# Performance work log

Hardware: AMD Instinct MI355X
Metric: run time of the kernel (lower is better)

Reference implementation:

```python
import jax, jax.numpy as jnp
import numpy as np

E = 2048   # embed_dim
H = 16     # num query heads
D = E // H # head_dim = 128
B = 2
S = 2048


def setup_inputs() -> dict:
    key = jax.random.key(0)
    ks = jax.random.split(key, 12)
    sc = 0.02
    return {
        "input": jax.random.normal(ks[0], (B, S, E), jnp.float32),
        "kv": jax.random.normal(ks[1], (B, S, E), jnp.float32),
        "Wq": jax.random.normal(ks[2], (E, E), jnp.float32) * sc,
        "bq": jnp.zeros((E,), jnp.float32),
        "Wk": jax.random.normal(ks[3], (D, E), jnp.float32) * sc,
        "bk": jnp.zeros((D,), jnp.float32),
        "Wv": jax.random.normal(ks[4], (D, E), jnp.float32) * sc,
        "bv": jnp.zeros((D,), jnp.float32),
        "Wo": jax.random.normal(ks[5], (E, E), jnp.float32) * sc,
        "bo": jnp.zeros((E,), jnp.float32),
        "expanding_context": 0,
    }


def reference(input, kv, Wq, bq, Wk, bk, Wv, bv, Wo, bo, expanding_context):
    b, s, _ = input.shape
    # projections (torch Linear: x @ W.T + b)
    q = (input @ Wq.T + bq).reshape(b, s, H, D).transpose(0, 2, 1, 3)  # [B,H,S,D]
    k = kv @ Wk.T + bk  # [B,S,D] single KV head
    v = kv @ Wv.T + bv  # [B,S,D]
    # scores with single KV head broadcast across query heads
    scores = jnp.einsum('bhsd,btd->bhst', q, k) / jnp.sqrt(jnp.float32(D))
    causal = jnp.triu(jnp.ones((s, s), bool), k=1)  # True above diagonal
    scores = jnp.where(causal[None, None], jnp.float32(-jnp.inf), scores)
    attn = jax.nn.softmax(scores, axis=-1)
    out = jnp.einsum('bhst,btd->bhsd', attn, v)  # [B,H,S,D]
    out = out.transpose(0, 2, 1, 3).reshape(b, s, E)
    return out @ Wo.T + bo
```

## Files before the change

### kernel.cpp

```cpp
#include <hip/hip_runtime.h>

#define B_  2
#define S_  2048
#define E_  2048
#define H_  16
#define D_  128
#define BS_ (B_*S_)

typedef __bf16 bf16_t;
typedef __bf16 bf16x8 __attribute__((ext_vector_type(8)));
typedef __bf16 bf16x4 __attribute__((ext_vector_type(4)));
typedef float  f32x4  __attribute__((ext_vector_type(4)));
typedef float  f32x16 __attribute__((ext_vector_type(16)));

#define QSCALE 0.1275174131003543f

__device__ __forceinline__ void gld16(const bf16_t* g, bf16_t* l) {
    __builtin_amdgcn_global_load_lds(
        (const __attribute__((address_space(1))) void*)g,
        (__attribute__((address_space(3))) void*)l,
        16, 0, 0);
}

__global__ void cvt_all(const float* __restrict__ s0, const float* __restrict__ s1,
                        const float* __restrict__ s2, const float* __restrict__ s3,
                        const float* __restrict__ s4, const float* __restrict__ s5,
                        bf16_t* d0, bf16_t* d1, bf16_t* d2,
                        bf16_t* d3, bf16_t* d4, bf16_t* d5)
{
    long i = ((long)blockIdx.x * blockDim.x + threadIdx.x) * 4;
    const float* s; bf16_t* d;
    if      (i <  8388608) { s = s0; d = d0; }
    else if (i < 16777216) { s = s1; d = d1; i -=  8388608; }
    else if (i < 20971520) { s = s2; d = d2; i -= 16777216; }
    else if (i < 21233664) { s = s3; d = d3; i -= 20971520; }
    else if (i < 21495808) { s = s4; d = d4; i -= 21233664; }
    else                   { s = s5; d = d5; i -= 21495808; }
    float4 v = *(const float4*)(s + i);
    bf16x4 o;
    o[0] = (bf16_t)v.x; o[1] = (bf16_t)v.y; o[2] = (bf16_t)v.z; o[3] = (bf16_t)v.w;
    *(bf16x4*)(d + i) = o;
}

template<int EP>
__device__ __forceinline__ void gemm_tile128(
    const bf16_t* __restrict__ A, const bf16_t* __restrict__ W,
    const float* __restrict__ bias,
    bf16_t* __restrict__ Cb,
    int N, int K, int kb, int ke, float scale, int m0, int w_n0, int c_n0,
    bf16_t* As, bf16_t* Bs)
{
    const int tid  = threadIdx.x;
    const int wave = tid >> 6, lane = tid & 63;
    const int wm = wave >> 1, wn = wave & 1;
    const int lrow = lane & 15, quad = lane >> 4;
    const int r8 = lane >> 3, c8 = (lane & 7) << 3;

    f32x4 acc[4][4] = {};

    for (int k0 = kb; k0 < ke; k0 += 64) {
        __syncthreads();
#pragma unroll
        for (int j = 0; j < 4; ++j) {
            int base = (wave * 4 + j) * 8;
            gld16(A + (size_t)(m0 + base + r8) * K + k0 + c8, &As[base * 64]);
        }
#pragma unroll
        for (int j = 0; j < 4; ++j) {
            int base = (wave * 4 + j) * 8;
            gld16(W + (size_t)(w_n0 + base + r8) * K + k0 + c8, &Bs[base * 64]);
        }
        __syncthreads();
#pragma unroll
        for (int ks = 0; ks < 2; ++ks) {
            bf16x8 af[4], bfr[4];
#pragma unroll
            for (int mt = 0; mt < 4; ++mt)
                af[mt] = *(const bf16x8*)&As[(wm * 64 + mt * 16 + lrow) * 64 + ks * 32 + quad * 8];
#pragma unroll
            for (int nt = 0; nt < 4; ++nt)
                bfr[nt] = *(const bf16x8*)&Bs[(wn * 64 + nt * 16 + lrow) * 64 + ks * 32 + quad * 8];
#pragma unroll
            for (int mt = 0; mt < 4; ++mt)
#pragma unroll
                for (int nt = 0; nt < 4; ++nt)
                    acc[mt][nt] = __builtin_amdgcn_mfma_f32_16x16x32_bf16(
                        af[mt], bfr[nt], acc[mt][nt], 0, 0, 0);
        }
    }

#pragma unroll
    for (int mt = 0; mt < 4; ++mt) {
#pragma unroll
        for (int nt = 0; nt < 4; ++nt) {
            int lcol = wn * 64 + nt * 16 + lrow;
            int col = c_n0 + lcol;
            float bvv = (EP == 1) ? bias[lcol] : 0.f;
#pragma unroll
            for (int r = 0; r < 4; ++r) {
                int row = m0 + wm * 64 + mt * 16 + quad * 4 + r;
                float v = (EP == 1) ? (acc[mt][nt][r] + bvv) * scale
                                    : acc[mt][nt][r];
                Cb[(size_t)row * N + col] = (bf16_t)v;
            }
        }
    }
}

__global__ __launch_bounds__(256) void gemm_qkv(
    const bf16_t* __restrict__ xb, const bf16_t* __restrict__ kvb,
    const bf16_t* __restrict__ Wq, const bf16_t* __restrict__ Wkv,
    const float* __restrict__ bk, const float* __restrict__ bv,
    bf16_t* __restrict__ Qp0, bf16_t* __restrict__ Qp1,
    bf16_t* __restrict__ KVb)
{
    __shared__ __align__(16) bf16_t As[128 * 64];
    __shared__ __align__(16) bf16_t Bs[128 * 64];
    const int m0 = blockIdx.y * 128;
    const int x = blockIdx.x, z = blockIdx.z;
    if (x < 16) {
        int n0 = x * 128;
        bf16_t* Qz = z ? Qp1 : Qp0;
        gemm_tile128<2>(xb, Wq, nullptr, Qz, E_, E_,
                        z * 1024, z * 1024 + 1024, 1.0f, m0, n0, n0, As, Bs);
    } else if (z == 0) {
        if (x == 16)
            gemm_tile128<1>(kvb, Wkv, bk, KVb, 256, E_, 0, E_, 1.0f,
                            m0, 0, 0, As, Bs);
        else
            gemm_tile128<1>(kvb, Wkv, bv, KVb, 256, E_, 0, E_, 1.0f,
                            m0, 128, 128, As, Bs);
    }
}

__global__ __launch_bounds__(256) void gemm_o(
    const bf16_t* __restrict__ A, const bf16_t* __restrict__ W,
    bf16_t* __restrict__ Op0, bf16_t* __restrict__ Op1)
{
    __shared__ __align__(16) bf16_t As[128 * 64];
    __shared__ __align__(16) bf16_t Bs[128 * 64];
    const int n0 = blockIdx.x * 128, z = blockIdx.z;
    bf16_t* Oz = z ? Op1 : Op0;
    gemm_tile128<2>(A, W, nullptr, Oz, E_, E_,
                    z * 1024, z * 1024 + 1024, 1.0f,
                    blockIdx.y * 128, n0, n0, As, Bs);
}

__global__ __launch_bounds__(256) void merge_out(
    const bf16_t* __restrict__ p0, const bf16_t* __restrict__ p1,
    const float* __restrict__ bo, float* __restrict__ out)
{
    long i = ((long)blockIdx.x * blockDim.x + threadIdx.x) * 4;
    bf16x4 a = *(const bf16x4*)(p0 + i);
    bf16x4 b = *(const bf16x4*)(p1 + i);
    float4 bb = *(const float4*)(bo + (i & 2047));
    float4 o;
    o.x = (float)a[0] + (float)b[0] + bb.x;
    o.y = (float)a[1] + (float)b[1] + bb.y;
    o.z = (float)a[2] + (float)b[2] + bb.z;
    o.w = (float)a[3] + (float)b[3] + bb.w;
    *(float4*)(out + i) = o;
}

__global__ __launch_bounds__(256, 2) void mqa_attn(
    const bf16_t* __restrict__ Qp0, const bf16_t* __restrict__ Qp1,
    const float* __restrict__ bq,
    const bf16_t* __restrict__ KV, bf16_t* __restrict__ O)
{
    __shared__ __align__(16) bf16_t Kt[2][64][136];
    __shared__ __align__(16) bf16_t Vt[2][128][72];

    const int bx = blockIdx.x, h = blockIdx.y, b = blockIdx.z;
    const int qb = b ? bx : (15 - bx);
    const int tid = threadIdx.x, wave = tid >> 6, lane = tid & 63;
    const int ln = lane & 31, hi = lane >> 5;
    const int q0w = qb * 128 + wave * 32;

    const bf16_t* kvp = KV + (size_t)(b * S_) * 256;

    bf16x8 qf[8];
    {
        size_t off = ((size_t)(b * S_ + q0w + ln)) * E_ + h * D_ + hi * 8;
        const bf16_t* q0p = Qp0 + off;
        const bf16_t* q1p = Qp1 + off;
        const float* bqp = bq + h * D_ + hi * 8;
#pragma unroll
        for (int st = 0; st < 8; ++st) {
            bf16x8 a0 = *(const bf16x8*)(q0p + st * 16);
            bf16x8 a1 = *(const bf16x8*)(q1p + st * 16);
            float4 c0 = *(const float4*)(bqp + st * 16);
            float4 c1 = *(const float4*)(bqp + st * 16 + 4);
            const float* cb0 = (const float*)&c0;
            const float* cb1 = (const float*)&c1;
#pragma unroll
            for (int j = 0; j < 8; ++j) {
                float bb = (j < 4) ? cb0[j] : cb1[j - 4];
                qf[st][j] = (bf16_t)(((float)a0[j] + (float)a1[j] + bb) * QSCALE);
            }
        }
    }

    bf16x8 ones;
#pragma unroll
    for (int j = 0; j < 8; ++j) ones[j] = (bf16_t)1.0f;

    f32x16 oacc[4] = {};
    f32x16 racc = {};
    bf16x8 af[4] = {};

    const int NT = 2 * qb + 2;
    const int Tw = (q0w + 31) >> 6;

    bf16x8 kreg[4], vA[2], vB[2];
    auto loadKV = [&](int kt) {
        const int k0 = kt * 64;
#pragma unroll
        for (int i = 0; i < 4; ++i) {
            int c = tid + 256 * i;
            kreg[i] = *(const bf16x8*)(kvp + (size_t)(k0 + (c >> 4)) * 256 + ((c & 15) << 3));
        }
#pragma unroll
        for (int i = 0; i < 2; ++i) {
            int c = tid + 256 * i;
            int n = (c & 31) * 2, d0 = (c >> 5) << 3;
            const bf16_t* src = kvp + (size_t)(k0 + n) * 256 + 128 + d0;
            vA[i] = *(const bf16x8*)src;
            vB[i] = *(const bf16x8*)(src + 256);
        }
    };
    auto stageWrite = [&](int bb) {
#pragma unroll
        for (int i = 0; i < 4; ++i) {
            int c = tid + 256 * i;
            *(bf16x8*)&Kt[bb][c >> 4][(c & 15) << 3] = kreg[i];
        }
#pragma unroll
        for (int i = 0; i < 2; ++i) {
            int c = tid + 256 * i;
            int n = (c & 31) * 2, d0 = (c >> 5) << 3;
#pragma unroll
            for (int j = 0; j < 8; ++j) {
                union { bf16_t h[2]; unsigned u; } w2;
                w2.h[0] = vA[i][j]; w2.h[1] = vB[i][j];
                *(unsigned*)&Vt[bb][d0 + j][n] = w2.u;
            }
        }
    };
    auto doPV = [&](int vb) {
        __builtin_amdgcn_s_setprio(1);
#pragma unroll
        for (int ks = 0; ks < 4; ++ks)
#pragma unroll
            for (int dt = 0; dt < 4; ++dt) {
                bf16x8 vf = *(const bf16x8*)&Vt[vb][dt * 32 + ln][ks * 16 + hi * 8];
                oacc[dt] = __builtin_amdgcn_mfma_f32_32x32x16_bf16(af[ks], vf, oacc[dt], 0, 0, 0);
            }
        __builtin_amdgcn_s_setprio(0);
    };

    loadKV(0);
    stageWrite(0);
    if (NT > 1) loadKV(1);

    for (int t = 0; t < NT; ++t) {
        const int cur = t & 1;
        if (t >= 1 && t - 1 <= Tw) doPV(cur ^ 1);
        __syncthreads();
        if (t + 1 < NT) stageWrite(cur ^ 1);
        if (t + 2 < NT) loadKV(t + 2);
        if (t <= Tw) {
            f32x16 sc[2] = {f32x16{}, f32x16{}};
            __builtin_amdgcn_s_setprio(1);
#pragma unroll
            for (int st = 0; st < 8; ++st) {
                bf16x8 qv = qf[st];
#pragma unroll
                for (int ct = 0; ct < 2; ++ct) {
                    bf16x8 kf = *(const bf16x8*)&Kt[cur][ct * 32 + ln][st * 16 + hi * 8];
                    sc[ct] = __builtin_amdgcn_mfma_f32_32x32x16_bf16(kf, qv, sc[ct], 0, 0, 0);
                }
            }
            __builtin_amdgcn_s_setprio(0);
            const int k_base = t * 64;
            const int qi = q0w + ln;
            if (k_base + 63 > q0w) {
#pragma unroll
                for (int ct = 0; ct < 2; ++ct)
#pragma unroll
                    for (int r = 0; r < 16; ++r) {
                        int kj = k_base + ct * 32 + (r & 3) + 8 * (r >> 2) + 4 * hi;
                        float s = (kj > qi) ? -1e30f : sc[ct][r];
                        sc[ct][r] = exp2f(s);
                    }
            } else {
#pragma unroll
                for (int ct = 0; ct < 2; ++ct)
#pragma unroll
                    for (int r = 0; r < 16; ++r)
                        sc[ct][r] = exp2f(sc[ct][r]);
            }
#pragma unroll
            for (int ks = 0; ks < 4; ++ks) {
                const int c = ks >> 1, b8 = (ks & 1) * 8;
                union { bf16_t h[2]; unsigned u; } pk0, pk1, pk2, pk3;
                pk0.h[0] = (bf16_t)sc[c][b8 + 0]; pk0.h[1] = (bf16_t)sc[c][b8 + 1];
                pk1.h[0] = (bf16_t)sc[c][b8 + 2]; pk1.h[1] = (bf16_t)sc[c][b8 + 3];
                pk2.h[0] = (bf16_t)sc[c][b8 + 4]; pk2.h[1] = (bf16_t)sc[c][b8 + 5];
                pk3.h[0] = (bf16_t)sc[c][b8 + 6]; pk3.h[1] = (bf16_t)sc[c][b8 + 7];
                const unsigned U0 = pk0.u, U1 = pk1.u, U2 = pk2.u, U3 = pk3.u;
                const unsigned V0 = __shfl_xor(U0, 32);
                const unsigned V1 = __shfl_xor(U1, 32);
                const unsigned V2 = __shfl_xor(U2, 32);
                const unsigned V3 = __shfl_xor(U3, 32);
                union { unsigned u[4]; bf16x8 v; } W;
                W.u[0] = hi ? V2 : U0;
                W.u[1] = hi ? V3 : U1;
                W.u[2] = hi ? U2 : V0;
                W.u[3] = hi ? U3 : V1;
                af[ks] = W.v;
            }
#pragma unroll
            for (int ks = 0; ks < 4; ++ks)
                racc = __builtin_amdgcn_mfma_f32_32x32x16_bf16(af[ks], ones, racc, 0, 0, 0);
        }
    }
    if (Tw == NT - 1) doPV(1);

    float inv[16];
#pragma unroll
    for (int r = 0; r < 16; ++r) inv[r] = 1.0f / racc[r];
#pragma unroll
    for (int dt = 0; dt < 4; ++dt)
#pragma unroll
        for (int r = 0; r < 16; ++r) {
            int ro = (r & 3) + 8 * (r >> 2) + 4 * hi;
            O[((size_t)(b * S_ + q0w + ro)) * E_ + h * D_ + dt * 32 + ln] =
                (bf16_t)(oacc[dt][r] * inv[r]);
        }
}

extern "C" void kernel_launch(void* const* d_in, const int* in_sizes, int n_in,
                              void* d_out, int out_size, void* d_ws, size_t ws_size,
                              hipStream_t stream)
{
    const float* x   = (const float*)d_in[0];
    const float* kv  = (const float*)d_in[1];
    const float* Wq  = (const float*)d_in[2];
    const float* bq  = (const float*)d_in[3];
    const float* Wk  = (const float*)d_in[4];
    const float* bk  = (const float*)d_in[5];
    const float* Wv  = (const float*)d_in[6];
    const float* bv  = (const float*)d_in[7];
    const float* Wo  = (const float*)d_in[8];
    const float* bo  = (const float*)d_in[9];
    float* out = (float*)d_out;

    bf16_t* p    = (bf16_t*)d_ws;
    bf16_t* xb   = p;  p += (size_t)BS_ * E_;
    bf16_t* kvb  = p;  p += (size_t)BS_ * E_;
    bf16_t* Wqb  = p;  p += (size_t)E_ * E_;
    bf16_t* Wkvb = p;  p += (size_t)2 * D_ * E_;
    bf16_t* Wob  = p;  p += (size_t)E_ * E_;
    bf16_t* Qp0  = p;  p += (size_t)BS_ * E_;
    bf16_t* KVb  = p;  p += (size_t)BS_ * 256;
    bf16_t* Ob   = p;  p += (size_t)BS_ * E_;
    bf16_t* Qp1  = p;  p += (size_t)BS_ * E_;

    cvt_all<<<dim3(25088), dim3(256), 0, stream>>>(
        x, kv, Wq, Wk, Wv, Wo,
        xb, kvb, Wqb, Wkvb, Wkvb + (size_t)D_ * E_, Wob);

    gemm_qkv<<<dim3(18, BS_ / 128, 2), 256, 0, stream>>>(
        xb, kvb, Wqb, Wkvb, bk, bv, Qp0, Qp1, KVb);

    mqa_attn<<<dim3(S_ / 128, H_, B_), 256, 0, stream>>>(Qp0, Qp1, bq, KVb, Ob);

    gemm_o<<<dim3(E_ / 128, BS_ / 128, 2), 256, 0, stream>>>(Ob, Wob, xb, kvb);

    merge_out<<<dim3(8192), dim3(256), 0, stream>>>(xb, kvb, bo, out);
}
```

Baseline: 352.6 us.

## Enlarge projection GEMM tiles to 256x256 with 512-thread blocks

Measured after the change: 404.7 us. 14.8% more time.

```diff
diff --git a/kernel.cpp b/kernel.cpp
--- a/kernel.cpp
+++ b/kernel.cpp
@@ -42,46 +42,46 @@
     *(bf16x4*)(d + i) = o;
 }
 
-template<int EP>
-__device__ __forceinline__ void gemm_tile128(
+template<int EP, int MREP>
+__device__ __forceinline__ void gemm_tile256(
     const bf16_t* __restrict__ A, const bf16_t* __restrict__ W,
-    const float* __restrict__ bias,
+    const float* __restrict__ biasA, const float* __restrict__ biasB,
     bf16_t* __restrict__ Cb,
     int N, int K, int kb, int ke, float scale, int m0, int w_n0, int c_n0,
     bf16_t* As, bf16_t* Bs)
 {
     const int tid  = threadIdx.x;
     const int wave = tid >> 6, lane = tid & 63;
-    const int wm = wave >> 1, wn = wave & 1;
+    const int wm = wave >> 2, wn = wave & 3;
     const int lrow = lane & 15, quad = lane >> 4;
     const int r8 = lane >> 3, c8 = (lane & 7) << 3;
 
-    f32x4 acc[4][4] = {};
+    f32x4 acc[MREP][4] = {};
 
     for (int k0 = kb; k0 < ke; k0 += 64) {
         __syncthreads();
 #pragma unroll
+        for (int j = 0; j < MREP / 2; ++j) {
+            int rbase = (wave * (MREP / 2) + j) * 8;
+            gld16(A + (size_t)(m0 + rbase + r8) * K + k0 + c8, &As[rbase * 64]);
+        }
+#pragma unroll
         for (int j = 0; j < 4; ++j) {
-            int base = (wave * 4 + j) * 8;
-            gld16(A + (size_t)(m0 + base + r8) * K + k0 + c8, &As[base * 64]);
-        }
-#pragma unroll
-        for (int j = 0; j < 4; ++j) {
-            int base = (wave * 4 + j) * 8;
-            gld16(W + (size_t)(w_n0 + base + r8) * K + k0 + c8, &Bs[base * 64]);
+            int rbase = (wave * 4 + j) * 8;
+            gld16(W + (size_t)(w_n0 + rbase + r8) * K + k0 + c8, &Bs[rbase * 64]);
         }
         __syncthreads();
 #pragma unroll
         for (int ks = 0; ks < 2; ++ks) {
-            bf16x8 af[4], bfr[4];
-#pragma unroll
-            for (int mt = 0; mt < 4; ++mt)
-                af[mt] = *(const bf16x8*)&As[(wm * 64 + mt * 16 + lrow) * 64 + ks * 32 + quad * 8];
+            bf16x8 af[MREP], bfr[4];
+#pragma unroll
+            for (int mt = 0; mt < MREP; ++mt)
+                af[mt] = *(const bf16x8*)&As[(wm * (MREP * 16) + mt * 16 + lrow) * 64 + ks * 32 + quad * 8];
 #pragma unroll
             for (int nt = 0; nt < 4; ++nt)
                 bfr[nt] = *(const bf16x8*)&Bs[(wn * 64 + nt * 16 + lrow) * 64 + ks * 32 + quad * 8];
 #pragma unroll
-            for (int mt = 0; mt < 4; ++mt)
+            for (int mt = 0; mt < MREP; ++mt)
 #pragma unroll
                 for (int nt = 0; nt < 4; ++nt)
                     acc[mt][nt] = __builtin_amdgcn_mfma_f32_16x16x32_bf16(
@@ -90,15 +90,16 @@
     }
 
 #pragma unroll
-    for (int mt = 0; mt < 4; ++mt) {
+    for (int mt = 0; mt < MREP; ++mt) {
 #pragma unroll
         for (int nt = 0; nt < 4; ++nt) {
             int lcol = wn * 64 + nt * 16 + lrow;
             int col = c_n0 + lcol;
-            float bvv = (EP == 1) ? bias[lcol] : 0.f;
+            float bvv = 0.f;
+            if (EP == 1) bvv = (biasB && lcol >= 128) ? biasB[lcol - 128] : biasA[lcol];
 #pragma unroll
             for (int r = 0; r < 4; ++r) {
-                int row = m0 + wm * 64 + mt * 16 + quad * 4 + r;
+                int row = m0 + wm * (MREP * 16) + mt * 16 + quad * 4 + r;
                 float v = (EP == 1) ? (acc[mt][nt][r] + bvv) * scale
                                     : acc[mt][nt][r];
                 Cb[(size_t)row * N + col] = (bf16_t)v;
@@ -107,43 +108,38 @@
     }
 }
 
-__global__ __launch_bounds__(256) void gemm_qkv(
+__global__ __launch_bounds__(512, 2) void gemm_qkv(
     const bf16_t* __restrict__ xb, const bf16_t* __restrict__ kvb,
     const bf16_t* __restrict__ Wq, const bf16_t* __restrict__ Wkv,
     const float* __restrict__ bk, const float* __restrict__ bv,
     bf16_t* __restrict__ Qp0, bf16_t* __restrict__ Qp1,
     bf16_t* __restrict__ KVb)
 {
-    __shared__ __align__(16) bf16_t As[128 * 64];
-    __shared__ __align__(16) bf16_t Bs[128 * 64];
-    const int m0 = blockIdx.y * 128;
-    const int x = blockIdx.x, z = blockIdx.z;
-    if (x < 16) {
-        int n0 = x * 128;
+    __shared__ __align__(16) bf16_t As[256 * 64];
+    __shared__ __align__(16) bf16_t Bs[256 * 64];
+    const int x = blockIdx.x, y = blockIdx.y, z = blockIdx.z;
+    if (x < 8) {
+        int n0 = x * 256;
         bf16_t* Qz = z ? Qp1 : Qp0;
-        gemm_tile128<2>(xb, Wq, nullptr, Qz, E_, E_,
-                        z * 1024, z * 1024 + 1024, 1.0f, m0, n0, n0, As, Bs);
-    } else if (z == 0) {
-        if (x == 16)
-            gemm_tile128<1>(kvb, Wkv, bk, KVb, 256, E_, 0, E_, 1.0f,
-                            m0, 0, 0, As, Bs);
-        else
-            gemm_tile128<1>(kvb, Wkv, bv, KVb, 256, E_, 0, E_, 1.0f,
-                            m0, 128, 128, As, Bs);
-    }
-}
-
-__global__ __launch_bounds__(256) void gemm_o(
+        gemm_tile256<2, 8>(xb, Wq, nullptr, nullptr, Qz, E_, E_,
+                           z * 1024, z * 1024 + 1024, 1.0f, y * 256, n0, n0, As, Bs);
+    } else {
+        gemm_tile256<1, 4>(kvb, Wkv, bk, bv, KVb, 256, E_,
+                           0, E_, 1.0f, y * 256 + z * 128, 0, 0, As, Bs);
+    }
+}
+
+__global__ __launch_bounds__(512, 2) void gemm_o(
     const bf16_t* __restrict__ A, const bf16_t* __restrict__ W,
     bf16_t* __restrict__ Op0, bf16_t* __restrict__ Op1)
 {
-    __shared__ __align__(16) bf16_t As[128 * 64];
-    __shared__ __align__(16) bf16_t Bs[128 * 64];
-    const int n0 = blockIdx.x * 128, z = blockIdx.z;
+    __shared__ __align__(16) bf16_t As[256 * 64];
+    __shared__ __align__(16) bf16_t Bs[256 * 64];
+    const int n0 = blockIdx.x * 256, z = blockIdx.z;
     bf16_t* Oz = z ? Op1 : Op0;
-    gemm_tile128<2>(A, W, nullptr, Oz, E_, E_,
-                    z * 1024, z * 1024 + 1024, 1.0f,
-                    blockIdx.y * 128, n0, n0, As, Bs);
+    gemm_tile256<2, 8>(A, W, nullptr, nullptr, Oz, E_, E_,
+                       z * 1024, z * 1024 + 1024, 1.0f,
+                       blockIdx.y * 256, n0, n0, As, Bs);
 }
 
 __global__ __launch_bounds__(256) void merge_out(
@@ -370,12 +366,12 @@
         x, kv, Wq, Wk, Wv, Wo,
         xb, kvb, Wqb, Wkvb, Wkvb + (size_t)D_ * E_, Wob);
 
-    gemm_qkv<<<dim3(18, BS_ / 128, 2), 256, 0, stream>>>(
+    gemm_qkv<<<dim3(9, 16, 2), 512, 0, stream>>>(
         xb, kvb, Wqb, Wkvb, bk, bv, Qp0, Qp1, KVb);
 
     mqa_attn<<<dim3(S_ / 128, H_, B_), 256, 0, stream>>>(Qp0, Qp1, bq, KVb, Ob);
 
-    gemm_o<<<dim3(E_ / 128, BS_ / 128, 2), 256, 0, stream>>>(Ob, Wob, xb, kvb);
+    gemm_o<<<dim3(8, 16, 2), 512, 0, stream>>>(Ob, Wob, xb, kvb);
 
     merge_out<<<dim3(8192), dim3(256), 0, stream>>>(xb, kvb, bo, out);
 }
```
